# Kernel tuning notes

Measured on AMD Instinct MI355X. Metric: run time of the kernel, lower is better.

## Reference

```python
import jax, jax.numpy as jnp
import numpy as np
import math

B, S, H, N = 64, 512, 768, 16
C_COMP, C_REL = 5, 3
P = N * (N - 1)
LN_EPS = 1e-5

# ordered pair indices (i, j), i != j, row-major like the torch double loop
_PAIR_I, _PAIR_J = np.nonzero(~np.eye(N, dtype=bool))
_PAIR_I = jnp.asarray(_PAIR_I)
_PAIR_J = jnp.asarray(_PAIR_J)


def setup_inputs() -> dict:
    key = jax.random.key(0)
    ks = jax.random.split(key, 20)
    sc = 0.02
    p = lambda k, shape: (jax.random.normal(k, shape, jnp.float32) * sc)
    return {
        "last_hidden_state": jax.random.normal(ks[0], (B, S, H), jnp.float32),
        "span_starts": jax.random.randint(ks[1], (B, N), 0, 480).astype(jnp.int32),
        "span_lengths": jax.random.randint(ks[2], (B, N), 0, 31).astype(jnp.int32),
        "components": jax.random.randint(ks[3], (B, N), 0, C_COMP).astype(jnp.int32),
        "relations": jax.random.randint(ks[4], (B, P), 0, C_REL).astype(jnp.int32),
        # comp_classifier: Linear(H,512) -> Tanh -> Linear(512,C_COMP)
        "comp_w1": p(ks[5], (H, 512)), "comp_b1": jnp.zeros((512,), jnp.float32),
        "comp_w2": p(ks[6], (512, C_COMP)), "comp_b2": jnp.zeros((C_COMP,), jnp.float32),
        # Attention(H, H), no bias
        "wq": p(ks[7], (H, H)), "wk": p(ks[8], (H, H)), "wv": p(ks[9], (H, H)),
        # LayerNorm(H)
        "ln_g": jnp.ones((H,), jnp.float32), "ln_b": jnp.zeros((H,), jnp.float32),
        # rel_classifier: Linear(2H,512) -> Tanh -> Linear(512,C_REL)
        "rel_w1": p(ks[10], (2 * H, 512)), "rel_b1": jnp.zeros((512,), jnp.float32),
        "rel_w2": p(ks[11], (512, C_REL)), "rel_b2": jnp.zeros((C_REL,), jnp.float32),
    }


def _ce_mean(logits, gold):
    # logits [M, C], gold [M] -> scalar mean cross entropy
    logp = jax.nn.log_softmax(logits, axis=-1)
    return -jnp.mean(jnp.take_along_axis(logp, gold[:, None].astype(jnp.int32), axis=-1))


def reference(last_hidden_state, span_starts, span_lengths, components, relations,
              comp_w1, comp_b1, comp_w2, comp_b2,
              wq, wk, wv, ln_g, ln_b,
              rel_w1, rel_b1, rel_w2, rel_b2):
    # --- per-span mean pooling (inclusive end = start + length), masked+vectorized ---
    pos = jnp.arange(S)
    ends = span_starts + span_lengths
    mask = ((pos[None, None, :] >= span_starts[:, :, None]) &
            (pos[None, None, :] <= ends[:, :, None])).astype(jnp.float32)  # [B,N,S]
    lens = (span_lengths + 1).astype(jnp.float32)
    pooled = jnp.einsum('bns,bsh->bnh', mask, last_hidden_state) / lens[:, :, None]  # [B,N,H]
    # dropout(p=0.2) is identity in eval mode

    # --- component classifier ---
    comp_logits = jnp.tanh(pooled @ comp_w1 + comp_b1) @ comp_w2 + comp_b2  # [B,N,C_COMP]

    # --- small self-attention over spans ---
    q = pooled @ wq; k = pooled @ wk; v = pooled @ wv
    scores = jax.nn.softmax(jnp.einsum('bnd,bmd->bnm', q, k) / math.sqrt(H), axis=-1)
    attn = jnp.einsum('bnm,bmh->bnh', scores, v)

    # --- residual + layernorm ---
    x = pooled + attn
    mu = jnp.mean(x, axis=-1, keepdims=True)
    var = jnp.mean((x - mu) ** 2, axis=-1, keepdims=True)
    x = (x - mu) * jax.lax.rsqrt(var + LN_EPS) * ln_g + ln_b  # [B,N,H]

    # --- O(N^2) pairwise relation classification (ordered pairs i != j) ---
    pair_feat = jnp.concatenate([x[:, _PAIR_I, :], x[:, _PAIR_J, :]], axis=-1)  # [B,P,2H]
    rel_logits = jnp.tanh(pair_feat @ rel_w1 + rel_b1) @ rel_w2 + rel_b2  # [B,P,C_REL]

    loss_comp = _ce_mean(comp_logits.reshape(-1, C_COMP), components.reshape(-1))
    loss_rel = _ce_mean(rel_logits.reshape(-1, C_REL), relations.reshape(-1))
    return (comp_logits.reshape(-1, C_COMP), rel_logits.reshape(-1, C_REL), loss_comp, loss_rel)
```

## Files before the change

kernel.cpp:

```cpp
#include <hip/hip_runtime.h>

#define BB 64
#define SS 512
#define HH 768
#define NSPAN 16
#define PP 240
#define CCOMP 5
#define CREL 3

typedef unsigned short u16;
typedef __attribute__((ext_vector_type(8))) short bf16x8;
typedef __attribute__((ext_vector_type(4))) float f32x4;

__device__ __forceinline__ u16 f2bf(float f) {
    union { float f; unsigned int i; } v; v.f = f;
    unsigned int x = v.i;
    unsigned int lsb = (x >> 16) & 1u;
    x += 0x7fffu + lsb;
    return (u16)(x >> 16);
}

__device__ __forceinline__ float ftanh(float x) {
    float xc = fminf(fmaxf(x, -15.f), 15.f);
    float e = __expf(2.f * xc);
    return (e - 1.f) / (e + 1.f);
}

__global__ __launch_bounds__(256) void prep_kernel(
    const float* __restrict__ cw1, const float* __restrict__ wq,
    const float* __restrict__ wk, const float* __restrict__ wv,
    const float* __restrict__ rw1, u16* __restrict__ wcat_t, u16* __restrict__ relw_t) {
    int blk = blockIdx.x;
    const float* W; int ldw, nt; u16* outp;
    if (blk < 384)        {             W = cw1; ldw = 512; nt = 16; outp = wcat_t; }
    else if (blk < 960)   { blk -= 384; W = wq;  ldw = 768; nt = 24; outp = wcat_t + (size_t)512 * 768; }
    else if (blk < 1536)  { blk -= 960; W = wk;  ldw = 768; nt = 24; outp = wcat_t + (size_t)1280 * 768; }
    else if (blk < 2112)  { blk -= 1536; W = wv; ldw = 768; nt = 24; outp = wcat_t + (size_t)2048 * 768; }
    else if (blk < 2496)  { blk -= 2112; W = rw1; ldw = 512; nt = 16; outp = relw_t; }
    else                  { blk -= 2496; W = rw1 + (size_t)768 * 512; ldw = 512; nt = 16; outp = relw_t + (size_t)512 * 768; }
    int tk = blk / nt, tn = blk % nt;
    int k0 = tk * 32, n0 = tn * 32;
    __shared__ u16 Ls[32][36];
    int tid = threadIdx.x;
    int tx = tid & 31, ty = tid >> 5;
#pragma unroll
    for (int r = 0; r < 4; ++r) {
        int k = ty + r * 8;
        Ls[tx][k] = f2bf(W[(size_t)(k0 + k) * ldw + n0 + tx]);
    }
    __syncthreads();
#pragma unroll
    for (int r = 0; r < 4; ++r) {
        int n = ty + r * 8;
        outp[(size_t)(n0 + n) * 768 + k0 + tx] = Ls[n][tx];
    }
}

__global__ __launch_bounds__(256) void pool_kernel(
    const float* __restrict__ lhs, const int* __restrict__ starts,
    const int* __restrict__ lens, float* __restrict__ pooled, u16* __restrict__ pooled_bf) {
    int bn = blockIdx.x;
    int b = bn >> 4;
    int st = starts[bn];
    int ln = lens[bn];
    int tid = threadIdx.x;
    const float* base = lhs + ((size_t)b * SS + st) * HH;
    float a0 = 0.f, a1 = 0.f, a2 = 0.f;
    for (int s = 0; s <= ln; ++s) {
        const float* row = base + (size_t)s * HH;
        a0 += row[tid];
        a1 += row[tid + 256];
        a2 += row[tid + 512];
    }
    float inv = 1.0f / (float)(ln + 1);
    a0 *= inv; a1 *= inv; a2 *= inv;
    float* out = pooled + (size_t)bn * HH;
    u16* outb = pooled_bf + (size_t)bn * HH;
    out[tid] = a0;       out[tid + 256] = a1;       out[tid + 512] = a2;
    outb[tid] = f2bf(a0); outb[tid + 256] = f2bf(a1); outb[tid + 512] = f2bf(a2);
}

__global__ __launch_bounds__(256) void gemm_pw_kernel(
    const u16* __restrict__ pooled_bf, const u16* __restrict__ wcat_t,
    const float* __restrict__ comp_b1, float* __restrict__ y2) {
    __shared__ u16 As[64][72];
    __shared__ u16 Bs[64][72];
    int ccol0 = blockIdx.x * 64;
    int row0 = blockIdx.y * 64;
    int act = (ccol0 < 512);
    int tid = threadIdx.x;
    int lane = tid & 63, w = tid >> 6;
    int q = lane >> 4, l15 = lane & 15;
    int wm = (w & 1) * 32, wn = (w >> 1) * 32;
    int r = tid >> 2, c0 = (tid & 3) * 16;
    const u16* ga = pooled_bf + (size_t)(row0 + r) * 768 + c0;
    const u16* gb = wcat_t + (size_t)(ccol0 + r) * 768 + c0;
    f32x4 acc[2][2];
#pragma unroll
    for (int i = 0; i < 2; ++i)
#pragma unroll
        for (int j = 0; j < 2; ++j) acc[i][j] = (f32x4){0.f, 0.f, 0.f, 0.f};

    uint4 va0 = *(const uint4*)(ga);
    uint4 va1 = *(const uint4*)(ga + 8);
    uint4 vb0 = *(const uint4*)(gb);
    uint4 vb1 = *(const uint4*)(gb + 8);
    for (int k0 = 0; k0 < 768; k0 += 64) {
        __syncthreads();
        *(uint4*)(&As[r][c0]) = va0;
        *(uint4*)(&As[r][c0 + 8]) = va1;
        *(uint4*)(&Bs[r][c0]) = vb0;
        *(uint4*)(&Bs[r][c0 + 8]) = vb1;
        __syncthreads();
        if (k0 + 64 < 768) {
            va0 = *(const uint4*)(ga + k0 + 64);
            va1 = *(const uint4*)(ga + k0 + 72);
            vb0 = *(const uint4*)(gb + k0 + 64);
            vb1 = *(const uint4*)(gb + k0 + 72);
        }
#pragma unroll
        for (int ks = 0; ks < 2; ++ks) {
            bf16x8 a0 = *(const bf16x8*)(&As[wm + l15][ks * 32 + q * 8]);
            bf16x8 a1 = *(const bf16x8*)(&As[wm + 16 + l15][ks * 32 + q * 8]);
            bf16x8 b0 = *(const bf16x8*)(&Bs[wn + l15][ks * 32 + q * 8]);
            bf16x8 b1 = *(const bf16x8*)(&Bs[wn + 16 + l15][ks * 32 + q * 8]);
            acc[0][0] = __builtin_amdgcn_mfma_f32_16x16x32_bf16(a0, b0, acc[0][0], 0, 0, 0);
            acc[0][1] = __builtin_amdgcn_mfma_f32_16x16x32_bf16(a0, b1, acc[0][1], 0, 0, 0);
            acc[1][0] = __builtin_amdgcn_mfma_f32_16x16x32_bf16(a1, b0, acc[1][0], 0, 0, 0);
            acc[1][1] = __builtin_amdgcn_mfma_f32_16x16x32_bf16(a1, b1, acc[1][1], 0, 0, 0);
        }
    }
#pragma unroll
    for (int tm = 0; tm < 2; ++tm)
#pragma unroll
        for (int tn = 0; tn < 2; ++tn)
#pragma unroll
            for (int reg = 0; reg < 4; ++reg) {
                int rr = row0 + wm + tm * 16 + q * 4 + reg;
                int cc = ccol0 + wn + tn * 16 + l15;
                float v = acc[tm][tn][reg];
                if (act) v = ftanh(v + comp_b1[cc]);
                y2[(size_t)rr * 2816 + cc] = v;
            }
}

__global__ __launch_bounds__(256) void gemm_z_kernel(
    const u16* __restrict__ x_bf, const u16* __restrict__ relw_t, float* __restrict__ Z) {
    __shared__ u16 As[32][72];
    __shared__ u16 Bs[64][72];
    int ccol0 = blockIdx.x * 64;
    int row0 = blockIdx.y * 32;
    int tid = threadIdx.x;
    int lane = tid & 63, w = tid >> 6;
    int q = lane >> 4, l15 = lane & 15;
    int wm = (w & 1) * 16, wn = (w >> 1) * 32;
    int ra = tid >> 3, ca = (tid & 7) * 8;
    int rb = tid >> 2, cb = (tid & 3) * 16;
    const u16* ga = x_bf + (size_t)(row0 + ra) * 768 + ca;
    const u16* gb = relw_t + (size_t)(ccol0 + rb) * 768 + cb;
    f32x4 acc[2];
    acc[0] = (f32x4){0.f, 0.f, 0.f, 0.f};
    acc[1] = (f32x4){0.f, 0.f, 0.f, 0.f};

    uint4 va = *(const uint4*)(ga);
    uint4 vb0 = *(const uint4*)(gb);
    uint4 vb1 = *(const uint4*)(gb + 8);
    for (int k0 = 0; k0 < 768; k0 += 64) {
        __syncthreads();
        *(uint4*)(&As[ra][ca]) = va;
        *(uint4*)(&Bs[rb][cb]) = vb0;
        *(uint4*)(&Bs[rb][cb + 8]) = vb1;
        __syncthreads();
        if (k0 + 64 < 768) {
            va = *(const uint4*)(ga + k0 + 64);
            vb0 = *(const uint4*)(gb + k0 + 64);
            vb1 = *(const uint4*)(gb + k0 + 72);
        }
#pragma unroll
        for (int ks = 0; ks < 2; ++ks) {
            bf16x8 a0 = *(const bf16x8*)(&As[wm + l15][ks * 32 + q * 8]);
            bf16x8 b0 = *(const bf16x8*)(&Bs[wn + l15][ks * 32 + q * 8]);
            bf16x8 b1 = *(const bf16x8*)(&Bs[wn + 16 + l15][ks * 32 + q * 8]);
            acc[0] = __builtin_amdgcn_mfma_f32_16x16x32_bf16(a0, b0, acc[0], 0, 0, 0);
            acc[1] = __builtin_amdgcn_mfma_f32_16x16x32_bf16(a0, b1, acc[1], 0, 0, 0);
        }
    }
#pragma unroll
    for (int tn = 0; tn < 2; ++tn)
#pragma unroll
        for (int reg = 0; reg < 4; ++reg) {
            int rr = row0 + wm + q * 4 + reg;
            int cc = ccol0 + wn + tn * 16 + l15;
            Z[(size_t)rr * 1024 + cc] = acc[tn][reg];
        }
}

__global__ __launch_bounds__(256) void attn_ln_kernel(
    const float* __restrict__ y2, const float* __restrict__ pooled,
    const float* __restrict__ ln_g, const float* __restrict__ ln_b,
    u16* __restrict__ x_bf) {
    __shared__ float ks[16][772];
    __shared__ float Ssm[16][17];
    int b = blockIdx.x;
    int tid = threadIdx.x;
    int n = tid >> 4;
    int hl = tid & 15;

    for (int u = 0; u < 48; ++u) {
        int h = hl + (u << 4);
        ks[n][h] = y2[((size_t)(b * 16 + n)) * 2816 + 1280 + h];
    }
    __syncthreads();

    int m = tid & 15;
    const float* qrow = y2 + ((size_t)(b * 16 + n)) * 2816 + 512;
    float dot = 0.f;
    for (int h = 0; h < 768; h += 4) {
        float4 qv = *(const float4*)(qrow + h);
        float4 kv = *(const float4*)(&ks[m][h]);
        dot += qv.x * kv.x + qv.y * kv.y + qv.z * kv.z + qv.w * kv.w;
    }
    float sval = dot * 0.03608439182435161f;
    float mx = sval;
#pragma unroll
    for (int off = 8; off >= 1; off >>= 1) mx = fmaxf(mx, __shfl_xor(mx, off, 16));
    float pexp = __expf(sval - mx);
    float psum = pexp;
#pragma unroll
    for (int off = 8; off >= 1; off >>= 1) psum += __shfl_xor(psum, off, 16);
    Ssm[n][m] = pexp / psum;
    __syncthreads();

    for (int u = 0; u < 48; ++u) {
        int h = hl + (u << 4);
        ks[n][h] = y2[((size_t)(b * 16 + n)) * 2816 + 2048 + h];
    }
    __syncthreads();

    float sc[16];
#pragma unroll
    for (int mm = 0; mm < 16; ++mm) sc[mm] = Ssm[n][mm];
    int row = b * 16 + n;
    const float* prow = pooled + (size_t)row * HH;
    float xv[48];
    float ssum = 0.f, ssq = 0.f;
    for (int u = 0; u < 48; ++u) {
        int h = hl + (u << 4);
        float a = 0.f;
#pragma unroll
        for (int mm = 0; mm < 16; ++mm) a += sc[mm] * ks[mm][h];
        float v = prow[h] + a;
        xv[u] = v;
        ssum += v;
        ssq += v * v;
    }
#pragma unroll
    for (int off = 8; off >= 1; off >>= 1) {
        ssum += __shfl_xor(ssum, off, 16);
        ssq += __shfl_xor(ssq, off, 16);
    }
    float mu = ssum * (1.0f / 768.0f);
    float var = ssq * (1.0f / 768.0f) - mu * mu;
    float rs = rsqrtf(var + 1e-5f);
    u16* xrow_bf = x_bf + (size_t)row * HH;
    for (int u = 0; u < 48; ++u) {
        int h = hl + (u << 4);
        xrow_bf[h] = f2bf((xv[u] - mu) * rs * ln_g[h] + ln_b[h]);
    }
}

__global__ __launch_bounds__(256) void heads_kernel(
    const float* __restrict__ Z, const float* __restrict__ rb1,
    const float* __restrict__ rw2, const float* __restrict__ rb2,
    const int* __restrict__ rels,
    const float* __restrict__ y2, const float* __restrict__ cw2,
    const float* __restrict__ cb2, const int* __restrict__ comps,
    float* __restrict__ out, float* __restrict__ rel_p, float* __restrict__ comp_p) {
    __shared__ float red[4];
    int wave = threadIdx.x >> 6, lane = threadIdx.x & 63;
    if (blockIdx.x < 3840) {
        int row = blockIdx.x * 4 + wave;
        int b = row / PP;
        int p = row - b * PP;
        int i = p / 15;
        int jj = p - i * 15;
        int j = jj + (jj >= i ? 1 : 0);
        const float* z1 = Z + ((size_t)(b * 16 + i)) * 1024;
        const float* z2 = Z + ((size_t)(b * 16 + j)) * 1024 + 512;
        float a0 = 0.f, a1 = 0.f, a2 = 0.f;
#pragma unroll
        for (int t = 0; t < 8; ++t) {
            int c = lane + (t << 6);
            float h = ftanh(z1[c] + z2[c] + rb1[c]);
            a0 += h * rw2[c * 3 + 0];
            a1 += h * rw2[c * 3 + 1];
            a2 += h * rw2[c * 3 + 2];
        }
#pragma unroll
        for (int off = 32; off >= 1; off >>= 1) {
            a0 += __shfl_down(a0, off);
            a1 += __shfl_down(a1, off);
            a2 += __shfl_down(a2, off);
        }
        if (lane == 0) {
            float l0 = a0 + rb2[0];
            float l1 = a1 + rb2[1];
            float l2 = a2 + rb2[2];
            float mx = fmaxf(l0, fmaxf(l1, l2));
            float se = __expf(l0 - mx) + __expf(l1 - mx) + __expf(l2 - mx);
            float lse = __logf(se) + mx;
            int g = rels[row];
            float lg = (g == 0) ? l0 : ((g == 1) ? l1 : l2);
            red[wave] = lse - lg;
            float* o = out + 5120 + (size_t)row * 3;
            o[0] = l0; o[1] = l1; o[2] = l2;
        }
        __syncthreads();
        if (threadIdx.x == 0) rel_p[blockIdx.x] = red[0] + red[1] + red[2] + red[3];
    } else {
        int row = (blockIdx.x - 3840) * 4 + wave;
        const float* hrow = y2 + (size_t)row * 2816;
        float acc[CCOMP] = {0.f, 0.f, 0.f, 0.f, 0.f};
#pragma unroll
        for (int t = 0; t < 8; ++t) {
            int c = lane + (t << 6);
            float h = hrow[c];
#pragma unroll
            for (int cc = 0; cc < CCOMP; ++cc) acc[cc] += h * cw2[c * CCOMP + cc];
        }
#pragma unroll
        for (int cc = 0; cc < CCOMP; ++cc)
#pragma unroll
            for (int off = 32; off >= 1; off >>= 1) acc[cc] += __shfl_down(acc[cc], off);
        if (lane == 0) {
            float l[CCOMP];
            float mx = -1e30f;
#pragma unroll
            for (int cc = 0; cc < CCOMP; ++cc) { l[cc] = acc[cc] + cb2[cc]; mx = fmaxf(mx, l[cc]); }
            float se = 0.f;
#pragma unroll
            for (int cc = 0; cc < CCOMP; ++cc) se += __expf(l[cc] - mx);
            float lse = __logf(se) + mx;
            red[wave] = lse - l[comps[row]];
#pragma unroll
            for (int cc = 0; cc < CCOMP; ++cc) out[row * CCOMP + cc] = l[cc];
        }
        __syncthreads();
        if (threadIdx.x == 0) comp_p[blockIdx.x - 3840] = red[0] + red[1] + red[2] + red[3];
    }
}

__global__ __launch_bounds__(256) void finalize_kernel(
    const float* __restrict__ comp_p, const float* __restrict__ rel_p,
    float* __restrict__ out) {
    __shared__ float rc[4], rr[4];
    int tid = threadIdx.x;
    int wave = tid >> 6, lane = tid & 63;
    float sc = comp_p[tid];
    float sr = 0.f;
#pragma unroll
    for (int k = 0; k < 15; ++k) sr += rel_p[tid + k * 256];
#pragma unroll
    for (int off = 32; off >= 1; off >>= 1) {
        sc += __shfl_down(sc, off);
        sr += __shfl_down(sr, off);
    }
    if (lane == 0) { rc[wave] = sc; rr[wave] = sr; }
    __syncthreads();
    if (tid == 0) {
        out[51200] = (rc[0] + rc[1] + rc[2] + rc[3]) * (1.0f / 1024.0f);
        out[51201] = (rr[0] + rr[1] + rr[2] + rr[3]) * (1.0f / 15360.0f);
    }
}

extern "C" void kernel_launch(void* const* d_in, const int* in_sizes, int n_in,
                              void* d_out, int out_size, void* d_ws, size_t ws_size,
                              hipStream_t stream) {
    const float* lhs     = (const float*)d_in[0];
    const int* starts    = (const int*)d_in[1];
    const int* lens      = (const int*)d_in[2];
    const int* comps     = (const int*)d_in[3];
    const int* rels      = (const int*)d_in[4];
    const float* comp_w1 = (const float*)d_in[5];
    const float* comp_b1 = (const float*)d_in[6];
    const float* comp_w2 = (const float*)d_in[7];
    const float* comp_b2 = (const float*)d_in[8];
    const float* wq      = (const float*)d_in[9];
    const float* wk      = (const float*)d_in[10];
    const float* wv      = (const float*)d_in[11];
    const float* ln_g    = (const float*)d_in[12];
    const float* ln_b    = (const float*)d_in[13];
    const float* rel_w1  = (const float*)d_in[14];
    const float* rel_b1  = (const float*)d_in[15];
    const float* rel_w2  = (const float*)d_in[16];
    const float* rel_b2  = (const float*)d_in[17];
    float* out = (float*)d_out;
    float* ws = (float*)d_ws;

    float* pooled = ws;
    float* y2     = pooled + 786432;
    float* Z      = y2 + 2883584;
    float* comp_p = Z + 1048576;
    float* rel_p  = comp_p + 256;
    u16* pooled_bf = (u16*)(rel_p + 3840);
    u16* x_bf      = pooled_bf + 786432;
    u16* wcat_t    = x_bf + 786432;
    u16* relw_t    = wcat_t + 2162688;

    prep_kernel<<<2880, 256, 0, stream>>>(comp_w1, wq, wk, wv, rel_w1, wcat_t, relw_t);
    pool_kernel<<<1024, 256, 0, stream>>>(lhs, starts, lens, pooled, pooled_bf);
    gemm_pw_kernel<<<dim3(44, 16), 256, 0, stream>>>(pooled_bf, wcat_t, comp_b1, y2);
    attn_ln_kernel<<<64, 256, 0, stream>>>(y2, pooled, ln_g, ln_b, x_bf);
    gemm_z_kernel<<<dim3(16, 32), 256, 0, stream>>>(x_bf, relw_t, Z);
    heads_kernel<<<4096, 256, 0, stream>>>(Z, rel_b1, rel_w2, rel_b2, rels,
                                           y2, comp_w2, comp_b2, comps,
                                           out, rel_p, comp_p);
    finalize_kernel<<<1, 256, 0, stream>>>(comp_p, rel_p, out);
}
```

Baseline: 243.2 us.

## Merge prep and pool kernels, enlarge GEMM row tile, stage Z in LDS for heads

Weight transpose/convert and span pooling now share one launch, which removes a kernel boundary so the two independent jobs can overlap. The pooled×weights GEMM tile grows from 64 to 128 rows, with each wave covering all 64 columns, which halves the grid and reuses B tiles more. The relation head loads each batch's 16 Z rows plus rel_w2 and rel_b1 into LDS once per block and loops over 60 pairs per block. This replaces per-pair global reads, and finalize reduces over fewer partials. The cost is less parallelism: 256 rel blocks with about 70KB of LDS each, and a 352-block GEMM.

```diff
diff --git a/kernel.cpp b/kernel.cpp
--- a/kernel.cpp
+++ b/kernel.cpp
@@ -26,95 +26,101 @@
     return (e - 1.f) / (e + 1.f);
 }
 
-__global__ __launch_bounds__(256) void prep_kernel(
+__global__ __launch_bounds__(256) void prep_pool_kernel(
     const float* __restrict__ cw1, const float* __restrict__ wq,
     const float* __restrict__ wk, const float* __restrict__ wv,
-    const float* __restrict__ rw1, u16* __restrict__ wcat_t, u16* __restrict__ relw_t) {
-    int blk = blockIdx.x;
-    const float* W; int ldw, nt; u16* outp;
-    if (blk < 384)        {             W = cw1; ldw = 512; nt = 16; outp = wcat_t; }
-    else if (blk < 960)   { blk -= 384; W = wq;  ldw = 768; nt = 24; outp = wcat_t + (size_t)512 * 768; }
-    else if (blk < 1536)  { blk -= 960; W = wk;  ldw = 768; nt = 24; outp = wcat_t + (size_t)1280 * 768; }
-    else if (blk < 2112)  { blk -= 1536; W = wv; ldw = 768; nt = 24; outp = wcat_t + (size_t)2048 * 768; }
-    else if (blk < 2496)  { blk -= 2112; W = rw1; ldw = 512; nt = 16; outp = relw_t; }
-    else                  { blk -= 2496; W = rw1 + (size_t)768 * 512; ldw = 512; nt = 16; outp = relw_t + (size_t)512 * 768; }
-    int tk = blk / nt, tn = blk % nt;
-    int k0 = tk * 32, n0 = tn * 32;
-    __shared__ u16 Ls[32][36];
-    int tid = threadIdx.x;
-    int tx = tid & 31, ty = tid >> 5;
-#pragma unroll
-    for (int r = 0; r < 4; ++r) {
-        int k = ty + r * 8;
-        Ls[tx][k] = f2bf(W[(size_t)(k0 + k) * ldw + n0 + tx]);
-    }
-    __syncthreads();
-#pragma unroll
-    for (int r = 0; r < 4; ++r) {
-        int n = ty + r * 8;
-        outp[(size_t)(n0 + n) * 768 + k0 + tx] = Ls[n][tx];
-    }
-}
-
-__global__ __launch_bounds__(256) void pool_kernel(
+    const float* __restrict__ rw1, u16* __restrict__ wcat_t, u16* __restrict__ relw_t,
     const float* __restrict__ lhs, const int* __restrict__ starts,
     const int* __restrict__ lens, float* __restrict__ pooled, u16* __restrict__ pooled_bf) {
-    int bn = blockIdx.x;
-    int b = bn >> 4;
-    int st = starts[bn];
-    int ln = lens[bn];
-    int tid = threadIdx.x;
-    const float* base = lhs + ((size_t)b * SS + st) * HH;
-    float a0 = 0.f, a1 = 0.f, a2 = 0.f;
-    for (int s = 0; s <= ln; ++s) {
-        const float* row = base + (size_t)s * HH;
-        a0 += row[tid];
-        a1 += row[tid + 256];
-        a2 += row[tid + 512];
-    }
-    float inv = 1.0f / (float)(ln + 1);
-    a0 *= inv; a1 *= inv; a2 *= inv;
-    float* out = pooled + (size_t)bn * HH;
-    u16* outb = pooled_bf + (size_t)bn * HH;
-    out[tid] = a0;       out[tid + 256] = a1;       out[tid + 512] = a2;
-    outb[tid] = f2bf(a0); outb[tid + 256] = f2bf(a1); outb[tid + 512] = f2bf(a2);
+    __shared__ u16 Ls[32][36];
+    int tid = threadIdx.x;
+    if (blockIdx.x < 2880) {
+        int blk = blockIdx.x;
+        const float* W; int ldw, nt; u16* outp;
+        if (blk < 384)        {             W = cw1; ldw = 512; nt = 16; outp = wcat_t; }
+        else if (blk < 960)   { blk -= 384; W = wq;  ldw = 768; nt = 24; outp = wcat_t + (size_t)512 * 768; }
+        else if (blk < 1536)  { blk -= 960; W = wk;  ldw = 768; nt = 24; outp = wcat_t + (size_t)1280 * 768; }
+        else if (blk < 2112)  { blk -= 1536; W = wv; ldw = 768; nt = 24; outp = wcat_t + (size_t)2048 * 768; }
+        else if (blk < 2496)  { blk -= 2112; W = rw1; ldw = 512; nt = 16; outp = relw_t; }
+        else                  { blk -= 2496; W = rw1 + (size_t)768 * 512; ldw = 512; nt = 16; outp = relw_t + (size_t)512 * 768; }
+        int tk = blk / nt, tn = blk % nt;
+        int k0 = tk * 32, n0 = tn * 32;
+        int tx = tid & 31, ty = tid >> 5;
+#pragma unroll
+        for (int r = 0; r < 4; ++r) {
+            int k = ty + r * 8;
+            Ls[tx][k] = f2bf(W[(size_t)(k0 + k) * ldw + n0 + tx]);
+        }
+        __syncthreads();
+#pragma unroll
+        for (int r = 0; r < 4; ++r) {
+            int n = ty + r * 8;
+            outp[(size_t)(n0 + n) * 768 + k0 + tx] = Ls[n][tx];
+        }
+    } else {
+        int bn = blockIdx.x - 2880;
+        int b = bn >> 4;
+        int st = starts[bn];
+        int ln = lens[bn];
+        const float* base = lhs + ((size_t)b * SS + st) * HH;
+        float a0 = 0.f, a1 = 0.f, a2 = 0.f;
+        for (int s = 0; s <= ln; ++s) {
+            const float* row = base + (size_t)s * HH;
+            a0 += row[tid];
+            a1 += row[tid + 256];
+            a2 += row[tid + 512];
+        }
+        float inv = 1.0f / (float)(ln + 1);
+        a0 *= inv; a1 *= inv; a2 *= inv;
+        float* out = pooled + (size_t)bn * HH;
+        u16* outb = pooled_bf + (size_t)bn * HH;
+        out[tid] = a0;       out[tid + 256] = a1;       out[tid + 512] = a2;
+        outb[tid] = f2bf(a0); outb[tid + 256] = f2bf(a1); outb[tid + 512] = f2bf(a2);
+    }
 }
 
 __global__ __launch_bounds__(256) void gemm_pw_kernel(
     const u16* __restrict__ pooled_bf, const u16* __restrict__ wcat_t,
     const float* __restrict__ comp_b1, float* __restrict__ y2) {
-    __shared__ u16 As[64][72];
+    __shared__ u16 As[128][72];
     __shared__ u16 Bs[64][72];
     int ccol0 = blockIdx.x * 64;
-    int row0 = blockIdx.y * 64;
+    int row0 = blockIdx.y * 128;
     int act = (ccol0 < 512);
     int tid = threadIdx.x;
     int lane = tid & 63, w = tid >> 6;
     int q = lane >> 4, l15 = lane & 15;
-    int wm = (w & 1) * 32, wn = (w >> 1) * 32;
+    int wm = w * 32;
     int r = tid >> 2, c0 = (tid & 3) * 16;
     const u16* ga = pooled_bf + (size_t)(row0 + r) * 768 + c0;
     const u16* gb = wcat_t + (size_t)(ccol0 + r) * 768 + c0;
-    f32x4 acc[2][2];
+    const u16* ga2 = ga + (size_t)64 * 768;
+    f32x4 acc[2][4];
 #pragma unroll
     for (int i = 0; i < 2; ++i)
 #pragma unroll
-        for (int j = 0; j < 2; ++j) acc[i][j] = (f32x4){0.f, 0.f, 0.f, 0.f};
-
-    uint4 va0 = *(const uint4*)(ga);
-    uint4 va1 = *(const uint4*)(ga + 8);
+        for (int j = 0; j < 4; ++j) acc[i][j] = (f32x4){0.f, 0.f, 0.f, 0.f};
+
+    uint4 va00 = *(const uint4*)(ga);
+    uint4 va01 = *(const uint4*)(ga + 8);
+    uint4 va10 = *(const uint4*)(ga2);
+    uint4 va11 = *(const uint4*)(ga2 + 8);
     uint4 vb0 = *(const uint4*)(gb);
     uint4 vb1 = *(const uint4*)(gb + 8);
     for (int k0 = 0; k0 < 768; k0 += 64) {
         __syncthreads();
-        *(uint4*)(&As[r][c0]) = va0;
-        *(uint4*)(&As[r][c0 + 8]) = va1;
+        *(uint4*)(&As[r][c0]) = va00;
+        *(uint4*)(&As[r][c0 + 8]) = va01;
+        *(uint4*)(&As[r + 64][c0]) = va10;
+        *(uint4*)(&As[r + 64][c0 + 8]) = va11;
         *(uint4*)(&Bs[r][c0]) = vb0;
         *(uint4*)(&Bs[r][c0 + 8]) = vb1;
         __syncthreads();
         if (k0 + 64 < 768) {
-            va0 = *(const uint4*)(ga + k0 + 64);
-            va1 = *(const uint4*)(ga + k0 + 72);
+            va00 = *(const uint4*)(ga + k0 + 64);
+            va01 = *(const uint4*)(ga + k0 + 72);
+            va10 = *(const uint4*)(ga2 + k0 + 64);
+            va11 = *(const uint4*)(ga2 + k0 + 72);
             vb0 = *(const uint4*)(gb + k0 + 64);
             vb1 = *(const uint4*)(gb + k0 + 72);
         }
@@ -122,22 +128,22 @@
         for (int ks = 0; ks < 2; ++ks) {
             bf16x8 a0 = *(const bf16x8*)(&As[wm + l15][ks * 32 + q * 8]);
             bf16x8 a1 = *(const bf16x8*)(&As[wm + 16 + l15][ks * 32 + q * 8]);
-            bf16x8 b0 = *(const bf16x8*)(&Bs[wn + l15][ks * 32 + q * 8]);
-            bf16x8 b1 = *(const bf16x8*)(&Bs[wn + 16 + l15][ks * 32 + q * 8]);
-            acc[0][0] = __builtin_amdgcn_mfma_f32_16x16x32_bf16(a0, b0, acc[0][0], 0, 0, 0);
-            acc[0][1] = __builtin_amdgcn_mfma_f32_16x16x32_bf16(a0, b1, acc[0][1], 0, 0, 0);
-            acc[1][0] = __builtin_amdgcn_mfma_f32_16x16x32_bf16(a1, b0, acc[1][0], 0, 0, 0);
-            acc[1][1] = __builtin_amdgcn_mfma_f32_16x16x32_bf16(a1, b1, acc[1][1], 0, 0, 0);
+#pragma unroll
+            for (int tn = 0; tn < 4; ++tn) {
+                bf16x8 bt = *(const bf16x8*)(&Bs[tn * 16 + l15][ks * 32 + q * 8]);
+                acc[0][tn] = __builtin_amdgcn_mfma_f32_16x16x32_bf16(a0, bt, acc[0][tn], 0, 0, 0);
+                acc[1][tn] = __builtin_amdgcn_mfma_f32_16x16x32_bf16(a1, bt, acc[1][tn], 0, 0, 0);
+            }
         }
     }
 #pragma unroll
     for (int tm = 0; tm < 2; ++tm)
 #pragma unroll
-        for (int tn = 0; tn < 2; ++tn)
+        for (int tn = 0; tn < 4; ++tn)
 #pragma unroll
             for (int reg = 0; reg < 4; ++reg) {
                 int rr = row0 + wm + tm * 16 + q * 4 + reg;
-                int cc = ccol0 + wn + tn * 16 + l15;
+                int cc = ccol0 + tn * 16 + l15;
                 float v = acc[tm][tn][reg];
                 if (act) v = ftanh(v + comp_b1[cc]);
                 y2[(size_t)rr * 2816 + cc] = v;
@@ -276,49 +282,67 @@
     const float* __restrict__ y2, const float* __restrict__ cw2,
     const float* __restrict__ cb2, const int* __restrict__ comps,
     float* __restrict__ out, float* __restrict__ rel_p, float* __restrict__ comp_p) {
+    __shared__ float Zs[16][1024];
+    __shared__ float rw2s[1536];
+    __shared__ float rb1s[512];
     __shared__ float red[4];
-    int wave = threadIdx.x >> 6, lane = threadIdx.x & 63;
-    if (blockIdx.x < 3840) {
-        int row = blockIdx.x * 4 + wave;
-        int b = row / PP;
-        int p = row - b * PP;
-        int i = p / 15;
-        int jj = p - i * 15;
-        int j = jj + (jj >= i ? 1 : 0);
-        const float* z1 = Z + ((size_t)(b * 16 + i)) * 1024;
-        const float* z2 = Z + ((size_t)(b * 16 + j)) * 1024 + 512;
-        float a0 = 0.f, a1 = 0.f, a2 = 0.f;
-#pragma unroll
-        for (int t = 0; t < 8; ++t) {
-            int c = lane + (t << 6);
-            float h = ftanh(z1[c] + z2[c] + rb1[c]);
-            a0 += h * rw2[c * 3 + 0];
-            a1 += h * rw2[c * 3 + 1];
-            a2 += h * rw2[c * 3 + 2];
-        }
-#pragma unroll
-        for (int off = 32; off >= 1; off >>= 1) {
-            a0 += __shfl_down(a0, off);
-            a1 += __shfl_down(a1, off);
-            a2 += __shfl_down(a2, off);
-        }
-        if (lane == 0) {
-            float l0 = a0 + rb2[0];
-            float l1 = a1 + rb2[1];
-            float l2 = a2 + rb2[2];
-            float mx = fmaxf(l0, fmaxf(l1, l2));
-            float se = __expf(l0 - mx) + __expf(l1 - mx) + __expf(l2 - mx);
-            float lse = __logf(se) + mx;
-            int g = rels[row];
-            float lg = (g == 0) ? l0 : ((g == 1) ? l1 : l2);
-            red[wave] = lse - lg;
-            float* o = out + 5120 + (size_t)row * 3;
-            o[0] = l0; o[1] = l1; o[2] = l2;
-        }
-        __syncthreads();
-        if (threadIdx.x == 0) rel_p[blockIdx.x] = red[0] + red[1] + red[2] + red[3];
+    int tid = threadIdx.x;
+    int wave = tid >> 6, lane = tid & 63;
+    if (blockIdx.x < 256) {
+        int b = blockIdx.x >> 2;
+        int quarter = blockIdx.x & 3;
+        const float* zb = Z + (size_t)(b * 16) * 1024;
+#pragma unroll
+        for (int u = 0; u < 16; ++u) {
+            *(float4*)(&Zs[u][tid * 4]) = *(const float4*)(zb + (size_t)u * 1024 + tid * 4);
+        }
+#pragma unroll
+        for (int u = 0; u < 6; ++u) rw2s[tid + u * 256] = rw2[tid + u * 256];
+        rb1s[tid] = rb1[tid];
+        rb1s[tid + 256] = rb1[tid + 256];
+        __syncthreads();
+
+        float lsum = 0.f;
+        for (int it = 0; it < 15; ++it) {
+            int p = quarter * 60 + wave * 15 + it;
+            int i = p / 15;
+            int jj = p - i * 15;
+            int j = jj + (jj >= i ? 1 : 0);
+            float a0 = 0.f, a1 = 0.f, a2 = 0.f;
+#pragma unroll
+            for (int t = 0; t < 8; ++t) {
+                int c = lane + (t << 6);
+                float h = ftanh(Zs[i][c] + Zs[j][512 + c] + rb1s[c]);
+                a0 += h * rw2s[c * 3 + 0];
+                a1 += h * rw2s[c * 3 + 1];
+                a2 += h * rw2s[c * 3 + 2];
+            }
+#pragma unroll
+            for (int off = 32; off >= 1; off >>= 1) {
+                a0 += __shfl_down(a0, off);
+                a1 += __shfl_down(a1, off);
+                a2 += __shfl_down(a2, off);
+            }
+            if (lane == 0) {
+                int row = b * PP + p;
+                float l0 = a0 + rb2[0];
+                float l1 = a1 + rb2[1];
+                float l2 = a2 + rb2[2];
+                float mx = fmaxf(l0, fmaxf(l1, l2));
+                float se = __expf(l0 - mx) + __expf(l1 - mx) + __expf(l2 - mx);
+                float lse = __logf(se) + mx;
+                int g = rels[row];
+                float lg = (g == 0) ? l0 : ((g == 1) ? l1 : l2);
+                lsum += lse - lg;
+                float* o = out + 5120 + (size_t)row * 3;
+                o[0] = l0; o[1] = l1; o[2] = l2;
+            }
+        }
+        if (lane == 0) red[wave] = lsum;
+        __syncthreads();
+        if (tid == 0) rel_p[blockIdx.x] = red[0] + red[1] + red[2] + red[3];
     } else {
-        int row = (blockIdx.x - 3840) * 4 + wave;
+        int row = (blockIdx.x - 256) * 4 + wave;
         const float* hrow = y2 + (size_t)row * 2816;
         float acc[CCOMP] = {0.f, 0.f, 0.f, 0.f, 0.f};
 #pragma unroll
@@ -346,7 +370,7 @@
             for (int cc = 0; cc < CCOMP; ++cc) out[row * CCOMP + cc] = l[cc];
         }
         __syncthreads();
-        if (threadIdx.x == 0) comp_p[blockIdx.x - 3840] = red[0] + red[1] + red[2] + red[3];
+        if (tid == 0) comp_p[blockIdx.x - 256] = red[0] + red[1] + red[2] + red[3];
     }
 }
 
@@ -357,9 +381,7 @@
     int tid = threadIdx.x;
     int wave = tid >> 6, lane = tid & 63;
     float sc = comp_p[tid];
-    float sr = 0.f;
-#pragma unroll
-    for (int k = 0; k < 15; ++k) sr += rel_p[tid + k * 256];
+    float sr = rel_p[tid];
 #pragma unroll
     for (int off = 32; off >= 1; off >>= 1) {
         sc += __shfl_down(sc, off);
@@ -402,18 +424,18 @@
     float* Z      = y2 + 2883584;
     float* comp_p = Z + 1048576;
     float* rel_p  = comp_p + 256;
-    u16* pooled_bf = (u16*)(rel_p + 3840);
+    u16* pooled_bf = (u16*)(rel_p + 256);
     u16* x_bf      = pooled_bf + 786432;
     u16* wcat_t    = x_bf + 786432;
     u16* relw_t    = wcat_t + 2162688;
 
-    prep_kernel<<<2880, 256, 0, stream>>>(comp_w1, wq, wk, wv, rel_w1, wcat_t, relw_t);
-    pool_kernel<<<1024, 256, 0, stream>>>(lhs, starts, lens, pooled, pooled_bf);
-    gemm_pw_kernel<<<dim3(44, 16), 256, 0, stream>>>(pooled_bf, wcat_t, comp_b1, y2);
+    prep_pool_kernel<<<3904, 256, 0, stream>>>(comp_w1, wq, wk, wv, rel_w1, wcat_t, relw_t,
+                                               lhs, starts, lens, pooled, pooled_bf);
+    gemm_pw_kernel<<<dim3(44, 8), 256, 0, stream>>>(pooled_bf, wcat_t, comp_b1, y2);
     attn_ln_kernel<<<64, 256, 0, stream>>>(y2, pooled, ln_g, ln_b, x_bf);
     gemm_z_kernel<<<dim3(16, 32), 256, 0, stream>>>(x_bf, relw_t, Z);
-    heads_kernel<<<4096, 256, 0, stream>>>(Z, rel_b1, rel_w2, rel_b2, rels,
-                                           y2, comp_w2, comp_b2, comps,
-                                           out, rel_p, comp_p);
+    heads_kernel<<<512, 256, 0, stream>>>(Z, rel_b1, rel_w2, rel_b2, rels,
+                                          y2, comp_w2, comp_b2, comps,
+                                          out, rel_p, comp_p);
     finalize_kernel<<<1, 256, 0, stream>>>(comp_p, rel_p, out);
 }
```

New measurement: 248.4 us. 2.1% more time.
